# Performance work log

Measured on AMD Instinct MI355X. Metric: run time of the kernel, lower is better.

The kernel has to match this reference:

```python
import jax, jax.numpy as jnp
import numpy as np

DIM = 2048
H = 16
DK = 128
DV = 128
KCONV = 4
EPS = 1e-6
B = 2
S = 2048
KD = H * DK  # 2048
VD = H * DV  # 2048


def setup_inputs() -> dict:
    key = jax.random.key(0)
    ks = jax.random.split(key, 16)
    sc = 0.02
    inp = {
        "x": jax.random.normal(ks[0], (B, S, DIM), dtype=jnp.float32),
        "Wq": jax.random.normal(ks[1], (KD, DIM), dtype=jnp.float32) * sc,
        "Wk": jax.random.normal(ks[2], (KD, DIM), dtype=jnp.float32) * sc,
        "Wv": jax.random.normal(ks[3], (VD, DIM), dtype=jnp.float32) * sc,
        "Wa": jax.random.normal(ks[4], (H, DIM), dtype=jnp.float32) * sc,
        "Wb": jax.random.normal(ks[5], (H, DIM), dtype=jnp.float32) * sc,
        "Wg": jax.random.normal(ks[6], (VD, DIM), dtype=jnp.float32) * sc,
        "Wo": jax.random.normal(ks[7], (DIM, VD), dtype=jnp.float32) * sc,
        "cw_q": jax.random.normal(ks[8], (KD, KCONV), dtype=jnp.float32) * 0.3,
        "cb_q": jnp.zeros((KD,), dtype=jnp.float32),
        "cw_k": jax.random.normal(ks[9], (KD, KCONV), dtype=jnp.float32) * 0.3,
        "cb_k": jnp.zeros((KD,), dtype=jnp.float32),
        "cw_v": jax.random.normal(ks[10], (VD, KCONV), dtype=jnp.float32) * 0.3,
        "cb_v": jnp.zeros((VD,), dtype=jnp.float32),
        "A_log": jnp.zeros((H,), dtype=jnp.float32),
        "dt_bias": jnp.zeros((H,), dtype=jnp.float32),
        "norm_w": jnp.ones((VD,), dtype=jnp.float32),
    }
    return inp


def _causal_conv(x, w, b):
    # x: [B, S, C]; w: [C, K]; b: [C]. Depthwise causal conv (zero init state) + SiLU.
    Bb, Ss, C = x.shape
    xp = jnp.pad(x, ((0, 0), (KCONV - 1, 0), (0, 0)))
    out = b
    for j in range(KCONV):
        out = out + xp[:, j:j + Ss, :] * w[:, j]
    return jax.nn.silu(out)


def _l2norm(x):
    n = jnp.sqrt(jnp.sum(x * x, axis=-1, keepdims=True))
    return x / jnp.maximum(n, 1e-12)


def _forward(x, Wq, Wk, Wv, Wa, Wb, Wg, Wo, cw_q, cb_q, cw_k, cb_k, cw_v, cb_v,
             A_log, dt_bias, norm_w):
    Bb, Ss, _ = x.shape
    q = _causal_conv(x @ Wq.T, cw_q, cb_q)  # [B,S,KD]
    k = _causal_conv(x @ Wk.T, cw_k, cb_k)
    v = _causal_conv(x @ Wv.T, cw_v, cb_v)

    a = x @ Wa.T  # [B,S,H]
    b = x @ Wb.T
    g = jnp.exp(-jnp.exp(A_log)[None, None, :] * jax.nn.softplus(a + dt_bias[None, None, :]))
    beta = jax.nn.sigmoid(b)

    q = _l2norm(q.reshape(Bb, Ss, H, DK))
    k = _l2norm(k.reshape(Bb, Ss, H, DK))
    v = v.reshape(Bb, Ss, H, DV)

    S0 = jnp.zeros((Bb, H, DK, DV), dtype=x.dtype)

    def step(Sstate, inputs):
        q_t, k_t, v_t, g_t, beta_t = inputs  # [B,H,DK],[B,H,DK],[B,H,DV],[B,H],[B,H]
        retrieved = jnp.einsum('bhkv,bhk->bhv', Sstate, k_t)
        error = v_t - g_t[..., None] * retrieved
        update = k_t[..., :, None] * (beta_t[..., None] * error)[..., None, :]
        Snew = g_t[..., None, None] * Sstate + update
        o_t = jnp.einsum('bhkv,bhk->bhv', Snew, q_t)
        return Snew, o_t

    # scan over time: move time axis to front
    xs = (q.transpose(1, 0, 2, 3), k.transpose(1, 0, 2, 3), v.transpose(1, 0, 2, 3),
          g.transpose(1, 0, 2), beta.transpose(1, 0, 2))
    _, o = jax.lax.scan(step, S0, xs)  # o: [S,B,H,DV]
    o = o.transpose(1, 0, 2, 3).reshape(Bb, Ss, VD)

    # RMSNorm
    o = o * jax.lax.rsqrt(jnp.mean(o * o, axis=-1, keepdims=True) + EPS) * norm_w
    o = o * jax.nn.silu(x @ Wg.T)
    return o @ Wo.T


def reference(x, Wq, Wk, Wv, Wa, Wb, Wg, Wo, cw_q, cb_q, cw_k, cb_k, cw_v, cb_v,
              A_log, dt_bias, norm_w):
    return _forward(x, Wq, Wk, Wv, Wa, Wb, Wg, Wo, cw_q, cb_q, cw_k, cb_k,
                    cw_v, cb_v, A_log, dt_bias, norm_w)
```

## Files before the change

kernel.cpp:

```cpp
#include <hip/hip_runtime.h>

#define S_LEN   2048
#define NH      16
#define DIM     2048
#define KD      2048
#define VD      2048
#define MB      1048576ull
#define CT      64
#define NC      32

typedef short  short8  __attribute__((ext_vector_type(8)));
typedef short  short4v __attribute__((ext_vector_type(4)));
typedef float  floatx4 __attribute__((ext_vector_type(4)));

#define MFMA(a, b, c) __builtin_amdgcn_mfma_f32_16x16x32_bf16((a), (b), (c), 0, 0, 0)

__device__ inline short f2bf(float x) {
    unsigned u = __float_as_uint(x);
    unsigned r = (u + 0x7fffu + ((u >> 16) & 1u)) >> 16;
    return (short)r;
}
__device__ inline float bf2f(short s) {
    return __uint_as_float(((unsigned)(unsigned short)s) << 16);
}
__device__ inline float silu_f(float x) { return x / (1.f + __expf(-x)); }

__device__ inline short8 neg8(short8 a) {
    unsigned* p = (unsigned*)&a;
    p[0] ^= 0x80008000u; p[1] ^= 0x80008000u;
    p[2] ^= 0x80008000u; p[3] ^= 0x80008000u;
    return a;
}

__device__ inline void load_lds16(const void* g, void* l) {
    __builtin_amdgcn_global_load_lds(
        (const __attribute__((address_space(1))) unsigned int*)g,
        (__attribute__((address_space(3))) unsigned int*)l, 16, 0, 0);
}

__device__ inline void store_c(float* C, size_t idx, float v) { C[idx] = v; }
__device__ inline void store_c(short* C, size_t idx, float v) { C[idx] = f2bf(v); }

__device__ __forceinline__ void lds_barrier() {
    asm volatile("s_waitcnt lgkmcnt(0)" ::: "memory");
    __builtin_amdgcn_s_barrier();
}

__device__ __forceinline__ void boundary_barrier() {
    asm volatile("s_waitcnt lgkmcnt(0)" ::: "memory");
    __builtin_amdgcn_s_barrier();
    asm volatile("" ::: "memory");
}

#define VM(n_) asm volatile("s_waitcnt vmcnt(" #n_ ")" ::: "memory");

__global__ __launch_bounds__(256) void cvt_all_kernel(
    const float* __restrict__ x,  const float* __restrict__ Wq,
    const float* __restrict__ Wk, const float* __restrict__ Wv,
    const float* __restrict__ Wg, const float* __restrict__ Wo,
    short* __restrict__ xb,  short* __restrict__ Wqb, short* __restrict__ Wkb,
    short* __restrict__ Wvb, short* __restrict__ Wgb, short* __restrict__ Wob) {
    const float* in; short* out; int n8;
    switch (blockIdx.y) {
        case 0:  in = x;  out = xb;  n8 = 1048576; break;
        case 1:  in = Wq; out = Wqb; n8 = 524288;  break;
        case 2:  in = Wk; out = Wkb; n8 = 524288;  break;
        case 3:  in = Wv; out = Wvb; n8 = 524288;  break;
        case 4:  in = Wg; out = Wgb; n8 = 524288;  break;
        default: in = Wo; out = Wob; n8 = 524288;  break;
    }
    int i = blockIdx.x * 256 + threadIdx.x;
    if (i >= n8) return;
    float4 a = ((const float4*)in)[2 * i];
    float4 b = ((const float4*)in)[2 * i + 1];
    short8 o;
    o[0] = f2bf(a.x); o[1] = f2bf(a.y); o[2] = f2bf(a.z); o[3] = f2bf(a.w);
    o[4] = f2bf(b.x); o[5] = f2bf(b.y); o[6] = f2bf(b.z); o[7] = f2bf(b.w);
    ((short8*)out)[i] = o;
}


#define STAGE8(s_, isB_)                                                     \
    {                                                                        \
        const char* gsrc = (isB_) ? (const char*)Bw : (const char*)A;        \
        int t0 = (isB_) ? n0 : m0;                                           \
        char* dbase = smem + ((s_) & 3) * 32768 + (isB_) * 16384;            \
        _Pragma("unroll")                                                    \
        for (int ld = 0; ld < 2; ++ld) {                                     \
            int ch = ld * 8 + wave;                                          \
            int Pl = (ch << 10) + (lane << 4);                               \
            int Q  = Pl ^ (((lane >> 3) & 3) << 4);                          \
            const char* src = gsrc + ((size_t)(t0 + (Q >> 6)) << 12)         \
                              + ((size_t)(s_) << 6) + (Q & 63);              \
            load_lds16(src, dbase + (ch << 10));                             \
        }                                                                    \
    }

#define RD_AF(dst_, s_, qm_)                                                 \
    {                                                                        \
        const char* sb_ = smem + ((s_) & 3) * 32768;                         \
        _Pragma("unroll")                                                    \
        for (int mf = 0; mf < 4; ++mf)                                       \
            dst_[mf] = *(const short8*)(sb_ +                                \
                ((rowA_base + (qm_) * 64 + mf * 16) << 6) + qsw);            \
    }

#define RD_BF(dst_, s_)                                                      \
    {                                                                        \
        const char* sb_ = smem + ((s_) & 3) * 32768 + 16384;                 \
        _Pragma("unroll")                                                    \
        for (int nf = 0; nf < 4; ++nf)                                       \
            dst_[nf] = *(const short8*)(sb_ +                                \
                ((rowB_base + nf * 16) << 6) + qsw);                         \
    }

#define MM(qm_, af_, bf_)                                                    \
    {                                                                        \
        __builtin_amdgcn_s_setprio(1);                                       \
        _Pragma("unroll")                                                    \
        for (int mf = 0; mf < 4; ++mf)                                       \
            _Pragma("unroll")                                                \
            for (int nf = 0; nf < 4; ++nf)                                   \
                acc[(qm_) * 4 + mf][nf] =                                    \
                    MFMA(af_[mf], bf_[nf], acc[(qm_) * 4 + mf][nf]);         \
        __builtin_amdgcn_s_setprio(0);                                       \
    }

template <typename OutT>
__device__ __forceinline__ void gemm8_tile(const short* __restrict__ A,
                                           const short* __restrict__ Bw,
                                           OutT* __restrict__ C, char* smem) {
    int x  = blockIdx.x;
    int xs = (x & 7) * 16 + (x >> 3);
    int m0 = (xs >> 3) * 256;
    int n0 = (xs & 7) * 256;
    int tid  = threadIdx.x;
    int wave = tid >> 6, lane = tid & 63;
    int l16  = lane & 15, quad = lane >> 4;
    int wm = wave >> 2, wn = wave & 3;
    int qsw = ((quad ^ ((l16 >> 1) & 3)) << 4);
    int rowA_base = wm * 128 + l16;
    int rowB_base = wn * 64 + l16;

    floatx4 acc[8][4];
#pragma unroll
    for (int i = 0; i < 8; ++i)
#pragma unroll
        for (int j = 0; j < 4; ++j) acc[i][j] = (floatx4){0.f, 0.f, 0.f, 0.f};
    short8 af0[4], af1[4], bfA[4], bfB[4];

    STAGE8(0, 0) STAGE8(0, 1)
    STAGE8(1, 0) STAGE8(1, 1)
    STAGE8(2, 0) STAGE8(2, 1)
    VM(8)
    boundary_barrier();
    RD_AF(af0, 0, 0) RD_BF(bfA, 0)

#pragma unroll 1
    for (int sp = 0; sp < 60; sp += 2) {
        STAGE8(sp + 3, 0)
        RD_AF(af1, sp, 1)
        MM(0, af0, bfA)
        STAGE8(sp + 3, 1)
        VM(8)
        boundary_barrier();
        RD_AF(af0, sp + 1, 0) RD_BF(bfB, sp + 1)
        MM(1, af1, bfA)
        STAGE8(sp + 4, 0)
        RD_AF(af1, sp + 1, 1)
        MM(0, af0, bfB)
        STAGE8(sp + 4, 1)
        VM(8)
        boundary_barrier();
        RD_AF(af0, sp + 2, 0) RD_BF(bfA, sp + 2)
        MM(1, af1, bfB)
    }

    STAGE8(63, 0)
    RD_AF(af1, 60, 1)
    MM(0, af0, bfA)
    STAGE8(63, 1)
    VM(8)
    boundary_barrier();
    RD_AF(af0, 61, 0) RD_BF(bfB, 61)
    MM(1, af1, bfA)
    RD_AF(af1, 61, 1)
    MM(0, af0, bfB)
    VM(4)
    boundary_barrier();
    RD_AF(af0, 62, 0) RD_BF(bfA, 62)
    MM(1, af1, bfB)
    RD_AF(af1, 62, 1)
    MM(0, af0, bfA)
    VM(0)
    boundary_barrier();
    RD_AF(af0, 63, 0) RD_BF(bfB, 63)
    MM(1, af1, bfA)
    RD_AF(af1, 63, 1)
    MM(0, af0, bfB)
    MM(1, af1, bfB)

#pragma unroll
    for (int i = 0; i < 8; ++i) {
        int row0 = m0 + wm * 128 + (i >> 2) * 64 + (i & 3) * 16 + quad * 4;
#pragma unroll
        for (int nf = 0; nf < 4; ++nf) {
            int col = n0 + wn * 64 + nf * 16 + l16;
#pragma unroll
            for (int r = 0; r < 4; ++r)
                store_c(C, (size_t)(row0 + r) * 2048 + col, acc[i][nf][r]);
        }
    }
}

__global__ __launch_bounds__(512, 2) void gemm8_qkvg(const short* __restrict__ A,
    const short* __restrict__ B0, const short* __restrict__ B1,
    const short* __restrict__ B2, const short* __restrict__ B3,
    short* __restrict__ C0, short* __restrict__ C1,
    short* __restrict__ C2, short* __restrict__ C3) {
    extern __shared__ char smem[];
    const short* Bw; short* C;
    switch (blockIdx.z) {
        case 0:  Bw = B0; C = C0; break;
        case 1:  Bw = B1; C = C1; break;
        case 2:  Bw = B2; C = C2; break;
        default: Bw = B3; C = C3; break;
    }
    gemm8_tile<short>(A, Bw, C, smem);
}

__global__ __launch_bounds__(512, 2) void gemm_out128(const short* __restrict__ A,
    const short* __restrict__ Bw, float* __restrict__ C) {
    extern __shared__ char smem[];
    int x   = blockIdx.x;
    int swz = (x & 7) * 32 + (x >> 3);
    int m0  = (swz >> 3) * 128;
    int n0  = (swz & 7) * 256;
    int tid = threadIdx.x;
    int wave = tid >> 6, lane = tid & 63;
    int l16 = lane & 15, quad = lane >> 4;
    int wm = wave >> 2, wn = wave & 3;
    int qsw = ((quad ^ ((l16 >> 1) & 3)) << 4);
    int rowA = wm * 64 + l16;
    int rowB = wn * 64 + l16;

    floatx4 acc[4][4];
#pragma unroll
    for (int i = 0; i < 4; ++i)
#pragma unroll
        for (int j = 0; j < 4; ++j) acc[i][j] = (floatx4){0.f, 0.f, 0.f, 0.f};
    short8 afA[4], bfA[4], afB[4], bfB[4];

#define STG128(s_)                                                            \
    {                                                                         \
        char* dbase = smem + ((s_) & 3) * 24576;                              \
        {                                                                     \
            int D = (wave << 10) + (lane << 4);                               \
            int Q = D ^ (((lane >> 3) & 3) << 4);                             \
            const char* src = (const char*)A + ((size_t)(m0 + (Q >> 6)) << 12)\
                              + ((size_t)(s_) << 6) + (Q & 63);               \
            load_lds16(src, dbase + (wave << 10));                            \
        }                                                                     \
        _Pragma("unroll")                                                     \
        for (int ld = 0; ld < 2; ++ld) {                                      \
            int D = (ld << 13) + (wave << 10) + (lane << 4);                  \
            int Q = D ^ (((lane >> 3) & 3) << 4);                             \
            const char* src = (const char*)Bw + ((size_t)(n0 + (Q >> 6)) << 12)\
                              + ((size_t)(s_) << 6) + (Q & 63);               \
            load_lds16(src, dbase + 8192 + (ld << 13) + (wave << 10));        \
        }                                                                     \
    }

#define RD128(af_, bf_, s_)                                                   \
    {                                                                         \
        const char* sb_ = smem + ((s_) & 3) * 24576;                          \
        _Pragma("unroll")                                                     \
        for (int f = 0; f < 4; ++f) {                                         \
            af_[f] = *(const short8*)(sb_ + ((rowA + f * 16) << 6) + qsw);    \
            bf_[f] = *(const short8*)(sb_ + 8192 + ((rowB + f * 16) << 6) + qsw); \
        }                                                                     \
    }

#define MM128(af_, bf_)                                                       \
    {                                                                         \
        __builtin_amdgcn_s_setprio(1);                                        \
        _Pragma("unroll")                                                     \
        for (int i = 0; i < 4; ++i)                                           \
            _Pragma("unroll")                                                 \
            for (int j = 0; j < 4; ++j)                                       \
                acc[i][j] = MFMA(af_[i], bf_[j], acc[i][j]);                  \
        __builtin_amdgcn_s_setprio(0);                                        \
    }

    STG128(0) STG128(1) STG128(2)
    VM(6)
    boundary_barrier();
    RD128(afA, bfA, 0)

#pragma unroll 1
    for (int s = 0; s < 60; s += 2) {
        STG128(s + 3)
        VM(6)
        boundary_barrier();
        RD128(afB, bfB, s + 1)
        MM128(afA, bfA)
        STG128(s + 4)
        VM(6)
        boundary_barrier();
        RD128(afA, bfA, s + 2)
        MM128(afB, bfB)
    }
    STG128(63)
    VM(6)
    boundary_barrier();
    RD128(afB, bfB, 61)
    MM128(afA, bfA)
    VM(3)
    boundary_barrier();
    RD128(afA, bfA, 62)
    MM128(afB, bfB)
    VM(0)
    boundary_barrier();
    RD128(afB, bfB, 63)
    MM128(afA, bfA)
    MM128(afB, bfB)

#pragma unroll
    for (int i = 0; i < 4; ++i) {
        int row0 = m0 + wm * 64 + i * 16 + quad * 4;
#pragma unroll
        for (int j = 0; j < 4; ++j) {
            int col = n0 + wn * 64 + j * 16 + l16;
#pragma unroll
            for (int r = 0; r < 4; ++r)
                C[(size_t)(row0 + r) * 2048 + col] = acc[i][j][r];
        }
    }
#undef STG128
#undef RD128
#undef MM128
}

__global__ __launch_bounds__(256) void ab_kernel(const float* __restrict__ x,
    const float* __restrict__ Wa, const float* __restrict__ Wb,
    const float* __restrict__ Alog, const float* __restrict__ dtb,
    float* __restrict__ gdec, float* __restrict__ beta) {
    int t = threadIdx.x;
    int wave = t >> 6, lane = t & 63;
    int l16 = lane & 15, grp = lane >> 4;
    int m0 = (blockIdx.x * 4 + wave) * 2;
    const float4* x0 = (const float4*)(x + (size_t)m0 * DIM);
    const float4* x1 = (const float4*)(x + (size_t)(m0 + 1) * DIM);

#pragma unroll 1
    for (int p = 0; p < 8; ++p) {
        int c = p * 4 + grp;
        const float4* wr = (const float4*)((c < 16) ? (Wa + (size_t)c * DIM)
                                                    : (Wb + (size_t)(c - 16) * DIM));
        float s0 = 0.f, s1 = 0.f;
#pragma unroll 8
        for (int j = 0; j < 32; ++j) {
            float4 wv = wr[j * 16 + l16];
            float4 a0 = x0[j * 16 + l16];
            float4 a1 = x1[j * 16 + l16];
            s0 += a0.x * wv.x + a0.y * wv.y + a0.z * wv.z + a0.w * wv.w;
            s1 += a1.x * wv.x + a1.y * wv.y + a1.z * wv.z + a1.w * wv.w;
        }
#pragma unroll
        for (int off = 1; off < 16; off <<= 1) {
            s0 += __shfl_xor(s0, off);
            s1 += __shfl_xor(s1, off);
        }
        if (l16 < 2) {
            int m = m0 + l16;
            float sv = l16 ? s1 : s0;
            if (c < 16) {
                float sp = sv + dtb[c];
                float softp = (sp > 20.f) ? sp : log1pf(expf(sp));
                gdec[(size_t)m * NH + c] = expf(-expf(Alog[c]) * softp);
            } else {
                beta[(size_t)m * NH + (c - 16)] = 1.f / (1.f + expf(-sv));
            }
        }
    }
}

__global__ __launch_bounds__(256) void conv_kernel(
    const short* __restrict__ qr, const short* __restrict__ kr, const short* __restrict__ vr,
    const float* __restrict__ cwq, const float* __restrict__ cbq,
    const float* __restrict__ cwk, const float* __restrict__ cbk,
    const float* __restrict__ cwv, const float* __restrict__ cbv,
    short* __restrict__ qn, short* __restrict__ kn, short* __restrict__ vc) {
    int gw   = blockIdx.x * 4 + (threadIdx.x >> 6);
    int lane = threadIdx.x & 63;
    int h  = gw & (NH - 1);
    int m  = gw >> 4;
    int tt = m & (S_LEN - 1);
    int c  = h * 128 + lane * 2;
    size_t rowbase = (size_t)m * KD + c;

    float4 wq0 = ((const float4*)cwq)[c], wq1 = ((const float4*)cwq)[c + 1];
    float4 wk0 = ((const float4*)cwk)[c], wk1 = ((const float4*)cwk)[c + 1];
    float4 wv0 = ((const float4*)cwv)[c], wv1 = ((const float4*)cwv)[c + 1];
    float q0 = cbq[c], q1 = cbq[c + 1];
    float k0 = cbk[c], k1 = cbk[c + 1];
    float v0 = cbv[c], v1 = cbv[c + 1];
    const float* wq0a = (const float*)&wq0; const float* wq1a = (const float*)&wq1;
    const float* wk0a = (const float*)&wk0; const float* wk1a = (const float*)&wk1;
    const float* wv0a = (const float*)&wv0; const float* wv1a = (const float*)&wv1;
#pragma unroll
    for (int j = 0; j < 4; ++j) {
        int ts = tt - 3 + j;
        if (ts >= 0) {
            long long rb = (long long)rowbase + (long long)(j - 3) * KD;
            unsigned uq = *(const unsigned*)(qr + rb);
            unsigned uk = *(const unsigned*)(kr + rb);
            unsigned uv = *(const unsigned*)(vr + rb);
            q0 += bf2f((short)(uq & 0xffff)) * wq0a[j]; q1 += bf2f((short)(uq >> 16)) * wq1a[j];
            k0 += bf2f((short)(uk & 0xffff)) * wk0a[j]; k1 += bf2f((short)(uk >> 16)) * wk1a[j];
            v0 += bf2f((short)(uv & 0xffff)) * wv0a[j]; v1 += bf2f((short)(uv >> 16)) * wv1a[j];
        }
    }
    q0 = silu_f(q0); q1 = silu_f(q1);
    k0 = silu_f(k0); k1 = silu_f(k1);
    v0 = silu_f(v0); v1 = silu_f(v1);

    float sq = q0 * q0 + q1 * q1;
    float sk = k0 * k0 + k1 * k1;
#pragma unroll
    for (int off = 1; off < 64; off <<= 1) {
        sq += __shfl_xor(sq, off);
        sk += __shfl_xor(sk, off);
    }
    float iq = 1.f / fmaxf(sqrtf(sq), 1e-12f);
    float ik = 1.f / fmaxf(sqrtf(sk), 1e-12f);
    unsigned oq = (unsigned)(unsigned short)f2bf(q0 * iq) | ((unsigned)(unsigned short)f2bf(q1 * iq) << 16);
    unsigned ok = (unsigned)(unsigned short)f2bf(k0 * ik) | ((unsigned)(unsigned short)f2bf(k1 * ik) << 16);
    unsigned ov = (unsigned)(unsigned short)f2bf(v0)      | ((unsigned)(unsigned short)f2bf(v1)      << 16);
    *(unsigned*)(qn + rowbase) = oq;
    *(unsigned*)(kn + rowbase) = ok;
    *(unsigned*)(vc + rowbase) = ov;
}

__global__ __launch_bounds__(256) void solve_kernel(
    const short* __restrict__ kn, const short* __restrict__ vn,
    const float* __restrict__ gdec, const float* __restrict__ beta,
    short* __restrict__ UvT, short* __restrict__ Tk) {
    __shared__ short Pn[64][72];
    __shared__ short Pt[64][72];
    __shared__ short UT[128][72];
    __shared__ float Ls[64];
    __shared__ float Bs[64];

    int wg   = blockIdx.x;
    int half = wg & 1;
    int c    = (wg >> 1) & 31;
    int bh   = wg >> 6;
    int b = bh >> 4, h = bh & 15;
    int tid = threadIdx.x;
    int wave = tid >> 6, lane = tid & 63;
    int quad = lane >> 4, l16 = lane & 15;

    const short* Kb = kn + ((size_t)(b * S_LEN + c * CT)) * KD + h * 128;
    const short* Vb = vn + ((size_t)(b * S_LEN + c * CT)) * KD + h * 128;

    if (wave == 0) {
        float lg = __logf(gdec[((size_t)(b * S_LEN + c * CT) + lane) * NH + h]);
#pragma unroll
        for (int off = 1; off < 64; off <<= 1) {
            float y = __shfl_up(lg, off);
            if (lane >= off) lg += y;
        }
        Ls[lane] = lg;
        Bs[lane] = beta[((size_t)(b * S_LEN + c * CT) + lane) * NH + h];
    }
    __syncthreads();

    {
        floatx4 acc[4];
#pragma unroll
        for (int i = 0; i < 4; ++i) acc[i] = (floatx4){0.f, 0.f, 0.f, 0.f};
        for (int ks = 0; ks < 4; ++ks) {
            short8 af = *(const short8*)(Kb + (size_t)(wave * 16 + l16) * KD + ks * 32 + quad * 8);
#pragma unroll
            for (int it = 0; it < 4; ++it) {
                short8 bf = *(const short8*)(Kb + (size_t)(it * 16 + l16) * KD + ks * 32 + quad * 8);
                acc[it] = MFMA(af, bf, acc[it]);
            }
        }
#pragma unroll
        for (int it = 0; it < 4; ++it) {
            int icol = it * 16 + l16;
#pragma unroll
            for (int r = 0; r < 4; ++r) {
                int trow = wave * 16 + quad * 4 + r;
                float v = 0.f;
                if (icol < trow) v = -Bs[trow] * __expf(Ls[trow] - Ls[icol]) * acc[it][r];
                short bv = f2bf(v);
                Pn[trow][icol] = bv;
                Pt[icol][trow] = bv;
            }
        }
    }

    {
        const short* src = half ? Kb : Vb;
        int tr = tid >> 2, seg = (tid & 3) * 32;
        float s = Bs[tr] * (half ? __expf(Ls[tr]) : 1.f);
#pragma unroll
        for (int j = 0; j < 4; ++j) {
            short8 d = *(const short8*)(src + (size_t)tr * KD + seg + j * 8);
#pragma unroll
            for (int e = 0; e < 8; ++e)
                UT[seg + j * 8 + e][tr] = f2bf(bf2f(d[e]) * s);
        }
    }
    __syncthreads();

    for (int iter = 0; iter < 6; ++iter) {
        floatx4 acc[8];
#pragma unroll
        for (int nt = 0; nt < 8; ++nt) {
            short4v u4 = *(const short4v*)&UT[nt * 16 + l16][wave * 16 + quad * 4];
            floatx4 a;
#pragma unroll
            for (int e = 0; e < 4; ++e) a[e] = bf2f(u4[e]);
            acc[nt] = a;
        }
        for (int ks = 0; ks < 2; ++ks) {
            short8 af = *(const short8*)&Pn[wave * 16 + l16][ks * 32 + quad * 8];
#pragma unroll
            for (int nt = 0; nt < 8; ++nt) {
                short8 bf = *(const short8*)&UT[nt * 16 + l16][ks * 32 + quad * 8];
                acc[nt] = MFMA(af, bf, acc[nt]);
            }
        }
        __syncthreads();
        if (iter < 5) {
#pragma unroll
            for (int nt = 0; nt < 8; ++nt) {
                short4v w4;
#pragma unroll
                for (int e = 0; e < 4; ++e) w4[e] = f2bf(acc[nt][e]);
                *(short4v*)&UT[nt * 16 + l16][wave * 16 + quad * 4] = w4;
            }
            floatx4 pacc[4];
#pragma unroll
            for (int it = 0; it < 4; ++it) pacc[it] = (floatx4){0.f, 0.f, 0.f, 0.f};
            for (int ks = 0; ks < 2; ++ks) {
                short8 paf = *(const short8*)&Pn[wave * 16 + l16][ks * 32 + quad * 8];
#pragma unroll
                for (int it = 0; it < 4; ++it) {
                    short8 pbf = *(const short8*)&Pt[it * 16 + l16][ks * 32 + quad * 8];
                    pacc[it] = MFMA(paf, pbf, pacc[it]);
                }
            }
            __syncthreads();
#pragma unroll
            for (int it = 0; it < 4; ++it) {
                int icol = it * 16 + l16;
#pragma unroll
                for (int r = 0; r < 4; ++r) {
                    int trow = wave * 16 + quad * 4 + r;
                    short bv = f2bf(pacc[it][r]);
                    Pn[trow][icol] = bv;
                    Pt[icol][trow] = bv;
                }
            }
            __syncthreads();
        } else {
            size_t cb = (size_t)(bh * NC + c);
            if (half == 0) {
                int usw = (((wave * 2 + (quad >> 1)) ^ (l16 & 7)) << 3) + ((quad & 1) << 2);
#pragma unroll
                for (int nt = 0; nt < 8; ++nt) {
                    short4v w4;
#pragma unroll
                    for (int e = 0; e < 4; ++e) w4[e] = f2bf(acc[nt][e]);
                    *(short4v*)(UvT + (cb * 128 + nt * 16 + l16) * 64 + usw) = w4;
                }
            } else {
#pragma unroll
                for (int nt = 0; nt < 8; ++nt)
#pragma unroll
                    for (int r = 0; r < 4; ++r) {
                        int trow = wave * 16 + quad * 4 + r;
                        int colsw = (((nt * 2 + (l16 >> 3)) ^ (trow & 7)) << 3) + (l16 & 7);
                        Tk[(cb * 64 + trow) * 128 + colsw] = f2bf(acc[nt][r]);
                    }
            }
        }
    }
}

__global__ __launch_bounds__(256) void prepb_kernel(
    const short* __restrict__ qn, const short* __restrict__ kn,
    const float* __restrict__ gdec,
    short* __restrict__ Wb_, short* __restrict__ Qg,
    short* __restrict__ KtT, float* __restrict__ gam63) {
    __shared__ short KT[128][72];
    __shared__ float Ls[64];
    int wg = blockIdx.x;
    int c = wg & 31, bh = wg >> 5;
    int b = bh >> 4, h = bh & 15;
    int tid = threadIdx.x, wave = tid >> 6, lane = tid & 63;
    int quad = lane >> 4, l16 = lane & 15;
    const short* Qb = qn + ((size_t)(b * S_LEN + c * CT)) * KD + h * 128;
    const short* Kb = kn + ((size_t)(b * S_LEN + c * CT)) * KD + h * 128;

    if (wave == 0) {
        float lg = __logf(gdec[((size_t)(b * S_LEN + c * CT) + lane) * NH + h]);
#pragma unroll
        for (int off = 1; off < 64; off <<= 1) {
            float y = __shfl_up(lg, off);
            if (lane >= off) lg += y;
        }
        Ls[lane] = lg;
    }
    __syncthreads();
    size_t cb = (size_t)(bh * NC + c);
    if (tid == 0) gam63[cb] = __expf(Ls[63]);

    {
        floatx4 acc[4];
#pragma unroll
        for (int i = 0; i < 4; ++i) acc[i] = (floatx4){0.f, 0.f, 0.f, 0.f};
        for (int ks = 0; ks < 4; ++ks) {
            short8 af = *(const short8*)(Qb + (size_t)(wave * 16 + l16) * KD + ks * 32 + quad * 8);
#pragma unroll
            for (int it = 0; it < 4; ++it) {
                short8 bf = *(const short8*)(Kb + (size_t)(it * 16 + l16) * KD + ks * 32 + quad * 8);
                acc[it] = MFMA(af, bf, acc[it]);
            }
        }
#pragma unroll
        for (int it = 0; it < 4; ++it) {
            int icol = it * 16 + l16;
#pragma unroll
            for (int r = 0; r < 4; ++r) {
                int trow = wave * 16 + quad * 4 + r;
                float v = (icol <= trow) ? __expf(Ls[trow] - Ls[icol]) * acc[it][r] : 0.f;
                int colsw = (((it * 2 + (l16 >> 3)) ^ (trow & 7)) << 3) + (l16 & 7);
                Wb_[(cb * 64 + trow) * 64 + colsw] = f2bf(v);
            }
        }
    }

    {
        int tr = tid >> 2, seg = (tid & 3) * 32;
        float sq = __expf(Ls[tr]);
        float sk = __expf(Ls[63] - Ls[tr]);
#pragma unroll
        for (int j = 0; j < 4; ++j) {
            short8 dq = *(const short8*)(Qb + (size_t)tr * KD + seg + j * 8);
            short8 dk = *(const short8*)(Kb + (size_t)tr * KD + seg + j * 8);
            short8 oq;
#pragma unroll
            for (int e = 0; e < 8; ++e) {
                oq[e] = f2bf(bf2f(dq[e]) * sq);
                KT[seg + j * 8 + e][tr] = f2bf(bf2f(dk[e]) * sk);
            }
            int ch = (tid & 3) * 4 + j;
            *(short8*)(Qg + (cb * 64 + tr) * 128 + ((ch ^ (tr & 7)) << 3)) = oq;
        }
    }
    __syncthreads();
    {
        int dk = tid >> 1, seg = (tid & 1) * 32;
#pragma unroll
        for (int j = 0; j < 4; ++j) {
            short8 v = *(const short8*)&KT[dk][seg + j * 8];
            int ch = (tid & 1) * 4 + j;
            *(short8*)(KtT + (cb * 128 + dk) * 64 + ((ch ^ (dk & 7)) << 3)) = v;
        }
    }
}

__global__ __launch_bounds__(256, 1) void seq_kernel(
    const short* __restrict__ UvT, const short* __restrict__ Tk,
    const short* __restrict__ Wb_, const short* __restrict__ Qg,
    const short* __restrict__ KtT, const float* __restrict__ gam63,
    short* __restrict__ ob) {
    extern __shared__ char smem[];
    const int BUF = 65536;
    const int TKO = 0, QGO = 16384, KTO = 32768, UVO = 49152, WO = 57344;
    short (*ST)[136] = (short (*)[136])(smem + 131072);
    short (*UTs)[72] = (short (*)[72])(smem + 131072 + 17408);

    int wg = blockIdx.x;
    int vh = wg & 1, bh = wg >> 1;
    int b = bh >> 4, h = bh & 15;
    int tid = threadIdx.x, wave = tid >> 6, lane = tid & 63;
    int quad = lane >> 4, l16 = lane & 15;
    int swk = l16 & 7;

    for (int i = tid; i < 64 * 136; i += 256) ((short*)(smem + 131072))[i] = 0;
    floatx4 sacc[8];
#pragma unroll
    for (int i = 0; i < 8; ++i) sacc[i] = (floatx4){0.f, 0.f, 0.f, 0.f};

    size_t cb0 = (size_t)bh * NC;
    int row16 = wave * 16 + l16;
    int chq[4];
#pragma unroll
    for (int ks = 0; ks < 4; ++ks) chq[ks] = (((ks * 4 + quad) ^ swk) << 4);
    int uvoff = (((wave * 2 + (quad >> 1)) ^ swk) << 4) + ((quad & 1) << 3);

#define STAGE_CHUNK(bsel_, c_)                                                       \
    {                                                                                \
        char* dst = smem + (bsel_) * BUF;                                            \
        size_t cbs = cb0 + (c_);                                                     \
        const char* gt = (const char*)Tk  + cbs * 16384 + wave * 1024 + lane * 16;   \
        const char* gq = (const char*)Qg  + cbs * 16384 + wave * 1024 + lane * 16;   \
        const char* gk = (const char*)KtT + cbs * 16384 + wave * 1024 + lane * 16;   \
        const char* gu = (const char*)UvT + cbs * 16384 + (size_t)vh * 8192 + wave * 1024 + lane * 16; \
        const char* gw = (const char*)Wb_ + cbs * 8192  + wave * 1024 + lane * 16;   \
        _Pragma("unroll")                                                            \
        for (int it = 0; it < 4; ++it) {                                             \
            load_lds16(gt + it * 4096, dst + TKO + it * 4096 + wave * 1024);         \
            load_lds16(gq + it * 4096, dst + QGO + it * 4096 + wave * 1024);         \
            load_lds16(gk + it * 4096, dst + KTO + it * 4096 + wave * 1024);         \
        }                                                                            \
        _Pragma("unroll")                                                            \
        for (int it = 0; it < 2; ++it) {                                             \
            load_lds16(gu + it * 4096, dst + UVO + it * 4096 + wave * 1024);         \
            load_lds16(gw + it * 4096, dst + WO  + it * 4096 + wave * 1024);         \
        }                                                                            \
    }

    STAGE_CHUNK(0, 0)
    float gamA = gam63[cb0];
    __syncthreads();

#pragma unroll 1
    for (int c = 0; c < NC; ++c) {
        float gamN = 0.f;
        if (c + 1 < NC) {
            gamN = gam63[cb0 + c + 1];
            STAGE_CHUNK((c + 1) & 1, c + 1)
        }
        const char* bufc = smem + (c & 1) * BUF;

        floatx4 uacc[4], oacc[4];
#pragma unroll
        for (int vt = 0; vt < 4; ++vt) {
            short4v u4 = *(const short4v*)(bufc + UVO + (vt * 16 + l16) * 128 + uvoff);
            floatx4 a;
#pragma unroll
            for (int e = 0; e < 4; ++e) a[e] = bf2f(u4[e]);
            uacc[vt] = a;
            oacc[vt] = (floatx4){0.f, 0.f, 0.f, 0.f};
        }
#pragma unroll
        for (int ks = 0; ks < 4; ++ks) {
            short8 tkf = *(const short8*)(bufc + TKO + row16 * 256 + chq[ks]);
            short8 qgf = *(const short8*)(bufc + QGO + row16 * 256 + chq[ks]);
            short8 afT = neg8(tkf);
#pragma unroll
            for (int vt = 0; vt < 4; ++vt) {
                short8 bf = *(const short8*)&ST[vt * 16 + l16][ks * 32 + quad * 8];
                uacc[vt] = MFMA(afT, bf, uacc[vt]);
                oacc[vt] = MFMA(qgf, bf, oacc[vt]);
            }
        }
#pragma unroll
        for (int vt = 0; vt < 4; ++vt) {
            short4v w4;
#pragma unroll
            for (int e = 0; e < 4; ++e) w4[e] = f2bf(uacc[vt][e]);
            *(short4v*)&UTs[vt * 16 + l16][wave * 16 + quad * 4] = w4;
        }
        lds_barrier();
#pragma unroll
        for (int ks = 0; ks < 2; ++ks) {
            short8 wf = *(const short8*)(bufc + WO + row16 * 128 + chq[ks]);
#pragma unroll
            for (int vt = 0; vt < 4; ++vt) {
                short8 bf = *(const short8*)&UTs[vt * 16 + l16][ks * 32 + quad * 8];
                oacc[vt] = MFMA(wf, bf, oacc[vt]);
            }
        }
#pragma unroll
        for (int vt = 0; vt < 4; ++vt)
#pragma unroll
            for (int r = 0; r < 4; ++r) {
                int m = b * S_LEN + c * CT + wave * 16 + quad * 4 + r;
                ob[(size_t)m * VD + h * 128 + vh * 64 + vt * 16 + l16] = f2bf(oacc[vt][r]);
            }
#pragma unroll
        for (int dt = 0; dt < 8; ++dt)
#pragma unroll
            for (int e = 0; e < 4; ++e) sacc[dt][e] *= gamA;
#pragma unroll
        for (int ks = 0; ks < 2; ++ks) {
            short8 af = *(const short8*)&UTs[wave * 16 + l16][ks * 32 + quad * 8];
#pragma unroll
            for (int dt = 0; dt < 8; ++dt) {
                short8 ktf = *(const short8*)(bufc + KTO + (dt * 16 + l16) * 128 + chq[ks]);
                sacc[dt] = MFMA(af, ktf, sacc[dt]);
            }
        }
#pragma unroll
        for (int dt = 0; dt < 8; ++dt)
#pragma unroll
            for (int r = 0; r < 4; ++r)
                ST[wave * 16 + quad * 4 + r][dt * 16 + l16] = f2bf(sacc[dt][r]);

        if (c + 1 < NC) {
            asm volatile("s_waitcnt lgkmcnt(0)" ::: "memory");
            VM(16)
            __builtin_amdgcn_s_barrier();
        }
        gamA = gamN;
    }
#undef STAGE_CHUNK
}

__global__ __launch_bounds__(256) void rms_gate_kernel(
    const short* __restrict__ o, const short* __restrict__ graw,
    const float* __restrict__ nw, short* __restrict__ og) {
    __shared__ float red[4];
    int m = blockIdx.x, t = threadIdx.x;
    short8 a = ((const short8*)(o + (size_t)m * VD))[t];
    float av[8];
#pragma unroll
    for (int i = 0; i < 8; ++i) av[i] = bf2f(a[i]);
    float ss = 0.f;
#pragma unroll
    for (int i = 0; i < 8; ++i) ss += av[i] * av[i];
#pragma unroll
    for (int off = 1; off < 64; off <<= 1) ss += __shfl_xor(ss, off);
    if ((t & 63) == 0) red[t >> 6] = ss;
    __syncthreads();
    float tot = red[0] + red[1] + red[2] + red[3];
    float sc = rsqrtf(tot * (1.f / VD) + 1e-6f);
    short8 gv = ((const short8*)(graw + (size_t)m * VD))[t];
    float4 n0 = ((const float4*)nw)[2 * t];
    float4 n1 = ((const float4*)nw)[2 * t + 1];
    const float* na = (const float*)&n0;
    const float* nb = (const float*)&n1;
    short8 ov;
#pragma unroll
    for (int i = 0; i < 4; ++i) ov[i]     = f2bf(av[i]     * sc * na[i] * silu_f(bf2f(gv[i])));
#pragma unroll
    for (int i = 0; i < 4; ++i) ov[i + 4] = f2bf(av[i + 4] * sc * nb[i] * silu_f(bf2f(gv[i + 4])));
    ((short8*)(og + (size_t)m * VD))[t] = ov;
}

extern "C" void kernel_launch(void* const* d_in, const int* in_sizes, int n_in,
                              void* d_out, int out_size, void* d_ws, size_t ws_size,
                              hipStream_t stream) {
    const float* x    = (const float*)d_in[0];
    const float* Wq   = (const float*)d_in[1];
    const float* Wk   = (const float*)d_in[2];
    const float* Wv   = (const float*)d_in[3];
    const float* Wa   = (const float*)d_in[4];
    const float* Wb   = (const float*)d_in[5];
    const float* Wg   = (const float*)d_in[6];
    const float* Wo   = (const float*)d_in[7];
    const float* cwq  = (const float*)d_in[8];
    const float* cbq  = (const float*)d_in[9];
    const float* cwk  = (const float*)d_in[10];
    const float* cbk  = (const float*)d_in[11];
    const float* cwv  = (const float*)d_in[12];
    const float* cbv  = (const float*)d_in[13];
    const float* Alog = (const float*)d_in[14];
    const float* dtb  = (const float*)d_in[15];
    const float* nw   = (const float*)d_in[16];

    char* ws = (char*)d_ws;
    short* Wob = (short*)(ws);
    short* xb  = (short*)(ws + 8 * MB);
    short* Wqb = (short*)(ws + 24 * MB);
    short* Wkb = (short*)(ws + 32 * MB);
    short* Wvb = (short*)(ws + 40 * MB);
    short* Wgb = (short*)(ws + 48 * MB);
    short* qrb = (short*)(ws + 56 * MB);
    short* krb = (short*)(ws + 72 * MB);
    short* vrb = (short*)(ws + 88 * MB);
    short* grb = (short*)(ws + 104 * MB);
    short* qnb = (short*)(ws + 8 * MB);
    short* knb = (short*)(ws + 24 * MB);
    short* vnb = (short*)(ws + 40 * MB);
    float* gdec = (float*)(ws + 120 * MB);
    float* beta = (float*)(ws + 120 * MB + 262144);
    short* ob  = qrb;
    short* ogb = krb;
    short* UvT  = (short*)(ws + 121 * MB);
    short* Tkb  = (short*)(ws + 137 * MB);
    short* Wbuf = (short*)(ws + 153 * MB);
    short* Qgb  = (short*)(ws + 161 * MB);
    short* KtT  = (short*)(ws + 177 * MB);
    float* gm63 = (float*)(ws + 193 * MB);

    static bool attr_done = false;
    if (!attr_done) {
        hipFuncSetAttribute((const void*)gemm8_qkvg,
                            hipFuncAttributeMaxDynamicSharedMemorySize, 131072);
        hipFuncSetAttribute((const void*)gemm_out128,
                            hipFuncAttributeMaxDynamicSharedMemorySize, 98304);
        hipFuncSetAttribute((const void*)seq_kernel,
                            hipFuncAttributeMaxDynamicSharedMemorySize, 157696);
        attr_done = true;
    }

    cvt_all_kernel<<<dim3(4096, 6), 256, 0, stream>>>(x, Wq, Wk, Wv, Wg, Wo,
                                                      xb, Wqb, Wkb, Wvb, Wgb, Wob);

    ab_kernel<<<512, 256, 0, stream>>>(x, Wa, Wb, Alog, dtb, gdec, beta);

    gemm8_qkvg<<<dim3(128, 1, 4), 512, 131072, stream>>>(xb, Wqb, Wkb, Wvb, Wgb,
                                                         qrb, krb, vrb, grb);

    conv_kernel<<<16384, 256, 0, stream>>>(qrb, krb, vrb,
                                           cwq, cbq, cwk, cbk, cwv, cbv, qnb, knb, vnb);

    solve_kernel<<<2048, 256, 0, stream>>>(knb, vnb, gdec, beta, UvT, Tkb);
    prepb_kernel<<<1024, 256, 0, stream>>>(qnb, knb, gdec, Wbuf, Qgb, KtT, gm63);
    seq_kernel<<<64, 256, 157696, stream>>>(UvT, Tkb, Wbuf, Qgb, KtT, gm63, ob);

    rms_gate_kernel<<<4096, 256, 0, stream>>>(ob, grb, nw, ogb);

    gemm_out128<<<256, 512, 98304, stream>>>(ogb, Wob, (float*)d_out);
}
```

Baseline: 632.9 us.

## Replace QKVG GEMM with 256x128 tile, triple-buffered LDS pipeline

Swaps the 256x256-tile, four-stage QKVG projection GEMM for a 256x128 tile with a three-buffer LDS ring (72 KB) and a simpler read-stage-compute loop. The grid doubles to 256 blocks per matrix, and launch bounds now ask for 4 blocks per CU, aiming at more occupancy and better load balance across CUs. In exchange each tile reuses its operands less, the pipeline is shallower, and register pressure under the new launch bounds could limit performance.

```diff
diff --git a/kernel.cpp b/kernel.cpp
--- a/kernel.cpp
+++ b/kernel.cpp
@@ -79,141 +79,101 @@
     ((short8*)out)[i] = o;
 }
 
-
-#define STAGE8(s_, isB_)                                                     \
+template <typename OutT>
+__device__ __forceinline__ void gemm96_tile(const short* __restrict__ A,
+                                            const short* __restrict__ Bw,
+                                            OutT* __restrict__ C, char* smem) {
+    int x   = blockIdx.x;
+    int swz = (x & 7) * 32 + (x >> 3);
+    int m0  = (swz >> 4) * 256;
+    int n0  = (swz & 15) * 128;
+    int tid = threadIdx.x;
+    int wave = tid >> 6, lane = tid & 63;
+    int l16 = lane & 15, quad = lane >> 4;
+    int wm = wave >> 1, wn = wave & 1;
+    int qsw = ((quad ^ ((l16 >> 1) & 3)) << 4);
+    int lvA = ((wm * 64 + l16) << 6) + qsw;
+    int lvB = ((wn * 64 + l16) << 6) + qsw;
+
+    int key = ((lane >> 3) & 3) << 4;
+    int D0 = (wave << 10) + (lane << 4);
+    int D1 = ((8 + wave) << 10) + (lane << 4);
+    int Q0 = D0 ^ key, Q1 = D1 ^ key;
+    const char* pA0 = (const char*)A  + ((size_t)(m0 + (Q0 >> 6)) << 12) + (Q0 & 63);
+    const char* pA1 = (const char*)A  + ((size_t)(m0 + (Q1 >> 6)) << 12) + (Q1 & 63);
+    const char* pB  = (const char*)Bw + ((size_t)(n0 + (Q0 >> 6)) << 12) + (Q0 & 63);
+    int dA0 = wave << 10, dA1 = (8 + wave) << 10, dB = 16384 + (wave << 10);
+
+    floatx4 acc[4][4];
+#pragma unroll
+    for (int i = 0; i < 4; ++i)
+#pragma unroll
+        for (int j = 0; j < 4; ++j) acc[i][j] = (floatx4){0.f, 0.f, 0.f, 0.f};
+    short8 af[4], bf[4];
+
+#define STG96(bufc_, sadd_)                                                   \
+    load_lds16(pA0 + (sadd_), smem + (bufc_) * 24576 + dA0);                  \
+    load_lds16(pA1 + (sadd_), smem + (bufc_) * 24576 + dA1);                  \
+    load_lds16(pB  + (sadd_), smem + (bufc_) * 24576 + dB);
+
+#define RD96(bufc_)                                                          \
     {                                                                        \
-        const char* gsrc = (isB_) ? (const char*)Bw : (const char*)A;        \
-        int t0 = (isB_) ? n0 : m0;                                           \
-        char* dbase = smem + ((s_) & 3) * 32768 + (isB_) * 16384;            \
+        const char* sb_ = smem + (bufc_) * 24576;                            \
         _Pragma("unroll")                                                    \
-        for (int ld = 0; ld < 2; ++ld) {                                     \
-            int ch = ld * 8 + wave;                                          \
-            int Pl = (ch << 10) + (lane << 4);                               \
-            int Q  = Pl ^ (((lane >> 3) & 3) << 4);                          \
-            const char* src = gsrc + ((size_t)(t0 + (Q >> 6)) << 12)         \
-                              + ((size_t)(s_) << 6) + (Q & 63);              \
-            load_lds16(src, dbase + (ch << 10));                             \
+        for (int f = 0; f < 4; ++f) {                                        \
+            af[f] = *(const short8*)(sb_ + lvA + f * 1024);                  \
+            bf[f] = *(const short8*)(sb_ + 16384 + lvB + f * 1024);          \
         }                                                                    \
     }
 
-#define RD_AF(dst_, s_, qm_)                                                 \
-    {                                                                        \
-        const char* sb_ = smem + ((s_) & 3) * 32768;                         \
+#define MM96()                                                               \
+    __builtin_amdgcn_s_setprio(1);                                           \
+    _Pragma("unroll")                                                        \
+    for (int i = 0; i < 4; ++i)                                              \
         _Pragma("unroll")                                                    \
-        for (int mf = 0; mf < 4; ++mf)                                       \
-            dst_[mf] = *(const short8*)(sb_ +                                \
-                ((rowA_base + (qm_) * 64 + mf * 16) << 6) + qsw);            \
-    }
-
-#define RD_BF(dst_, s_)                                                      \
-    {                                                                        \
-        const char* sb_ = smem + ((s_) & 3) * 32768 + 16384;                 \
-        _Pragma("unroll")                                                    \
-        for (int nf = 0; nf < 4; ++nf)                                       \
-            dst_[nf] = *(const short8*)(sb_ +                                \
-                ((rowB_base + nf * 16) << 6) + qsw);                         \
-    }
-
-#define MM(qm_, af_, bf_)                                                    \
-    {                                                                        \
-        __builtin_amdgcn_s_setprio(1);                                       \
-        _Pragma("unroll")                                                    \
-        for (int mf = 0; mf < 4; ++mf)                                       \
-            _Pragma("unroll")                                                \
-            for (int nf = 0; nf < 4; ++nf)                                   \
-                acc[(qm_) * 4 + mf][nf] =                                    \
-                    MFMA(af_[mf], bf_[nf], acc[(qm_) * 4 + mf][nf]);         \
-        __builtin_amdgcn_s_setprio(0);                                       \
-    }
-
-template <typename OutT>
-__device__ __forceinline__ void gemm8_tile(const short* __restrict__ A,
-                                           const short* __restrict__ Bw,
-                                           OutT* __restrict__ C, char* smem) {
-    int x  = blockIdx.x;
-    int xs = (x & 7) * 16 + (x >> 3);
-    int m0 = (xs >> 3) * 256;
-    int n0 = (xs & 7) * 256;
-    int tid  = threadIdx.x;
-    int wave = tid >> 6, lane = tid & 63;
-    int l16  = lane & 15, quad = lane >> 4;
-    int wm = wave >> 2, wn = wave & 3;
-    int qsw = ((quad ^ ((l16 >> 1) & 3)) << 4);
-    int rowA_base = wm * 128 + l16;
-    int rowB_base = wn * 64 + l16;
-
-    floatx4 acc[8][4];
-#pragma unroll
-    for (int i = 0; i < 8; ++i)
-#pragma unroll
-        for (int j = 0; j < 4; ++j) acc[i][j] = (floatx4){0.f, 0.f, 0.f, 0.f};
-    short8 af0[4], af1[4], bfA[4], bfB[4];
-
-    STAGE8(0, 0) STAGE8(0, 1)
-    STAGE8(1, 0) STAGE8(1, 1)
-    STAGE8(2, 0) STAGE8(2, 1)
-    VM(8)
+        for (int j = 0; j < 4; ++j)                                          \
+            acc[i][j] = MFMA(af[i], bf[j], acc[i][j]);                       \
+    __builtin_amdgcn_s_setprio(0);
+
+    STG96(0, 0) STG96(1, 64)
+    VM(3)
     boundary_barrier();
-    RD_AF(af0, 0, 0) RD_BF(bfA, 0)
 
 #pragma unroll 1
-    for (int sp = 0; sp < 60; sp += 2) {
-        STAGE8(sp + 3, 0)
-        RD_AF(af1, sp, 1)
-        MM(0, af0, bfA)
-        STAGE8(sp + 3, 1)
-        VM(8)
+    for (int it = 0; it < 20; ++it) {
+        RD96(0) STG96(2, 128) MM96() VM(3)
         boundary_barrier();
-        RD_AF(af0, sp + 1, 0) RD_BF(bfB, sp + 1)
-        MM(1, af1, bfA)
-        STAGE8(sp + 4, 0)
-        RD_AF(af1, sp + 1, 1)
-        MM(0, af0, bfB)
-        STAGE8(sp + 4, 1)
-        VM(8)
+        RD96(1) STG96(0, 192) MM96() VM(3)
         boundary_barrier();
-        RD_AF(af0, sp + 2, 0) RD_BF(bfA, sp + 2)
-        MM(1, af1, bfB)
-    }
-
-    STAGE8(63, 0)
-    RD_AF(af1, 60, 1)
-    MM(0, af0, bfA)
-    STAGE8(63, 1)
-    VM(8)
+        RD96(2) STG96(1, 256) MM96() VM(3)
+        boundary_barrier();
+        pA0 += 192; pA1 += 192; pB += 192;
+    }
+    RD96(0) STG96(2, 128) MM96() VM(3)
     boundary_barrier();
-    RD_AF(af0, 61, 0) RD_BF(bfB, 61)
-    MM(1, af1, bfA)
-    RD_AF(af1, 61, 1)
-    MM(0, af0, bfB)
-    VM(4)
+    RD96(1) STG96(0, 192) MM96() VM(3)
     boundary_barrier();
-    RD_AF(af0, 62, 0) RD_BF(bfA, 62)
-    MM(1, af1, bfB)
-    RD_AF(af1, 62, 1)
-    MM(0, af0, bfA)
-    VM(0)
+    RD96(2)               MM96() VM(0)
     boundary_barrier();
-    RD_AF(af0, 63, 0) RD_BF(bfB, 63)
-    MM(1, af1, bfA)
-    RD_AF(af1, 63, 1)
-    MM(0, af0, bfB)
-    MM(1, af1, bfB)
-
-#pragma unroll
-    for (int i = 0; i < 8; ++i) {
-        int row0 = m0 + wm * 128 + (i >> 2) * 64 + (i & 3) * 16 + quad * 4;
-#pragma unroll
-        for (int nf = 0; nf < 4; ++nf) {
-            int col = n0 + wn * 64 + nf * 16 + l16;
+    RD96(0)               MM96()
+
+#pragma unroll
+    for (int i = 0; i < 4; ++i) {
+        int row0 = m0 + wm * 64 + i * 16 + quad * 4;
+#pragma unroll
+        for (int j = 0; j < 4; ++j) {
+            int col = n0 + wn * 64 + j * 16 + l16;
 #pragma unroll
             for (int r = 0; r < 4; ++r)
-                store_c(C, (size_t)(row0 + r) * 2048 + col, acc[i][nf][r]);
-        }
-    }
-}
-
-__global__ __launch_bounds__(512, 2) void gemm8_qkvg(const short* __restrict__ A,
+                store_c(C, (size_t)(row0 + r) * 2048 + col, acc[i][j][r]);
+        }
+    }
+#undef STG96
+#undef RD96
+#undef MM96
+}
+
+__global__ __launch_bounds__(512, 4) void gemm96_qkvg(const short* __restrict__ A,
     const short* __restrict__ B0, const short* __restrict__ B1,
     const short* __restrict__ B2, const short* __restrict__ B3,
     short* __restrict__ C0, short* __restrict__ C1,
@@ -226,7 +186,7 @@
         case 2:  Bw = B2; C = C2; break;
         default: Bw = B3; C = C3; break;
     }
-    gemm8_tile<short>(A, Bw, C, smem);
+    gemm96_tile<short>(A, Bw, C, smem);
 }
 
 __global__ __launch_bounds__(512, 2) void gemm_out128(const short* __restrict__ A,
@@ -895,8 +855,8 @@
 
     static bool attr_done = false;
     if (!attr_done) {
-        hipFuncSetAttribute((const void*)gemm8_qkvg,
-                            hipFuncAttributeMaxDynamicSharedMemorySize, 131072);
+        hipFuncSetAttribute((const void*)gemm96_qkvg,
+                            hipFuncAttributeMaxDynamicSharedMemorySize, 73728);
         hipFuncSetAttribute((const void*)gemm_out128,
                             hipFuncAttributeMaxDynamicSharedMemorySize, 98304);
         hipFuncSetAttribute((const void*)seq_kernel,
@@ -909,7 +869,7 @@
 
     ab_kernel<<<512, 256, 0, stream>>>(x, Wa, Wb, Alog, dtb, gdec, beta);
 
-    gemm8_qkvg<<<dim3(128, 1, 4), 512, 131072, stream>>>(xb, Wqb, Wkb, Wvb, Wgb,
+    gemm96_qkvg<<<dim3(256, 1, 4), 512, 73728, stream>>>(xb, Wqb, Wkb, Wvb, Wgb,
                                                          qrb, krb, vrb, grb);
 
     conv_kernel<<<16384, 256, 0, stream>>>(qrb, krb, vrb,
```

Result: no change. 644.8 us (+1.9%).
